# Performance work log

Hardware: AMD Instinct MI355X
Metric: run time of the kernel (lower is better)

Reference implementation:

```python
import jax, jax.numpy as jnp
import numpy as np
import math

D_HEAD = 64
D_MODEL = 1024
N_HEADS = D_MODEL // D_HEAD
MAX_TOKENS = 2048
BATCH = 4
SEQ = 2048


def setup_inputs() -> dict:
    key = jax.random.key(0)
    k1, k2, k3, k4, k5 = jax.random.split(key, 5)
    residual_stream = jax.random.normal(k1, (BATCH, SEQ, D_MODEL), dtype=jnp.float32)
    # kaiming_normal_ (fan_in = d_model for [head, d_model, d_head] with default mode)
    std_qkv = math.sqrt(2.0 / D_MODEL)
    weight_query = jax.random.normal(k2, (N_HEADS, D_MODEL, D_HEAD), dtype=jnp.float32) * std_qkv
    weight_key = jax.random.normal(k3, (N_HEADS, D_MODEL, D_HEAD), dtype=jnp.float32) * std_qkv
    weight_value = jax.random.normal(k4, (N_HEADS, D_MODEL, D_HEAD), dtype=jnp.float32) * std_qkv
    # xavier_normal_ for [d_model, d_model]
    std_out = math.sqrt(2.0 / (D_MODEL + D_MODEL))
    weight_out = jax.random.normal(k5, (D_MODEL, D_MODEL), dtype=jnp.float32) * std_out
    return {
        "residual_stream": residual_stream,
        "weight_query": weight_query,
        "weight_key": weight_key,
        "weight_value": weight_value,
        "weight_out": weight_out,
    }


def reference(residual_stream, weight_query, weight_key, weight_value, weight_out):
    # residual_stream: [b, s, m]; weights: [h, m, d]
    q = jnp.einsum("bsm,hmd->bhsd", residual_stream, weight_query)
    k = jnp.einsum("bsm,hmd->bhsd", residual_stream, weight_key)
    v = jnp.einsum("bsm,hmd->bhsd", residual_stream, weight_value)
    scores = jnp.einsum("bhqd,bhkd->bhqk", q, k) / math.sqrt(D_HEAD)  # [b,h,s,s]
    n = scores.shape[-1]
    causal = jnp.tril(jnp.ones((n, n), dtype=bool))
    scores = jnp.where(causal, scores, -jnp.inf)
    attn = jax.nn.softmax(scores, axis=-1)
    out = jnp.einsum("bhqk,bhkd->bhqd", attn, v)  # [b,h,s,d]
    b, h, s, d = out.shape
    concat = out.transpose(0, 2, 1, 3).reshape(b, s, h * d)  # [b,s,m]
    return jnp.einsum("bsm,mn->bsn", concat, weight_out)
```

## Files before the change

### kernel.cpp

```cpp
#include <hip/hip_runtime.h>
#include <hip/hip_bf16.h>
#include <math.h>

#define BATCH 4
#define SEQ   2048
#define DM    1024
#define NH    16
#define DH    64

#define QSCALE 0.1803368801111204f

typedef __bf16 bf16x8 __attribute__((ext_vector_type(8)));
typedef __bf16 bf16x4 __attribute__((ext_vector_type(4)));
typedef float  f32x4  __attribute__((ext_vector_type(4)));

__device__ __forceinline__ bf16x8 load8f(const float* __restrict__ base, size_t idx) {
    const float4 a = *(const float4*)(base + idx);
    const float4 b = *(const float4*)(base + idx + 4);
    bf16x8 r;
    r[0] = (__bf16)a.x; r[1] = (__bf16)a.y; r[2] = (__bf16)a.z; r[3] = (__bf16)a.w;
    r[4] = (__bf16)b.x; r[5] = (__bf16)b.y; r[6] = (__bf16)b.z; r[7] = (__bf16)b.w;
    return r;
}

__global__ __launch_bounds__(256)
void xconv_kernel(const float* __restrict__ X, __bf16* __restrict__ Xb)
{
    size_t idx = ((size_t)blockIdx.x * 256 + threadIdx.x) * 8;
    *(bf16x8*)&Xb[idx] = load8f(X, idx);
}

__global__ __launch_bounds__(256)
void wtrans_kernel(const float* __restrict__ src, __bf16* __restrict__ dst,
                   int K, int N)
{
    const int k0 = blockIdx.x * 64;
    const int n0 = blockIdx.y * 64;
    src += (size_t)blockIdx.z * K * N;
    dst += (size_t)blockIdx.z * K * N;

    __shared__ __bf16 T[64][65];
    const int t = threadIdx.x;

#pragma unroll
    for (int i = 0; i < 4; ++i) {
        int row = i * 16 + (t >> 4);
        int col = (t & 15) * 4;
        float4 v = *(const float4*)&src[(size_t)(k0 + row) * N + n0 + col];
        T[col + 0][row] = (__bf16)v.x;
        T[col + 1][row] = (__bf16)v.y;
        T[col + 2][row] = (__bf16)v.z;
        T[col + 3][row] = (__bf16)v.w;
    }
    __syncthreads();
#pragma unroll
    for (int i = 0; i < 4; ++i) {
        int n  = i * 16 + (t >> 4);
        int kc = (t & 15) * 4;
        bf16x4 v;
        v[0] = T[n][kc + 0]; v[1] = T[n][kc + 1];
        v[2] = T[n][kc + 2]; v[3] = T[n][kc + 3];
        *(bf16x4*)&dst[(size_t)(n0 + n) * K + k0 + kc] = v;
    }
}

__global__ __launch_bounds__(256)
void qkv_kernel(const __bf16* __restrict__ Xb,
                const __bf16* __restrict__ Wqt,
                const __bf16* __restrict__ Wkt,
                const __bf16* __restrict__ Wvt,
                __bf16* __restrict__ Qo,
                __bf16* __restrict__ Ko,
                __bf16* __restrict__ Vto)
{
    const int rowTile = blockIdx.x;
    const int h       = blockIdx.y;
    const size_t woff = (size_t)h * DH * DM;

    __shared__ __align__(16) __bf16 As[128 * 40];
    __shared__ __align__(16) __bf16 Bq[64 * 40];
    __shared__ __align__(16) __bf16 Bk[64 * 40];
    __shared__ __align__(16) __bf16 Bv[64 * 40];

    const int t    = threadIdx.x;
    const int wave = t >> 6;
    const int lane = t & 63;
    const int l15  = lane & 15;
    const int quad = lane >> 4;

    f32x4 aq[2][4], ak[2][4], av[2][4];
#pragma unroll
    for (int s = 0; s < 2; ++s)
#pragma unroll
        for (int i = 0; i < 4; ++i) {
            aq[s][i] = (f32x4){0.f, 0.f, 0.f, 0.f};
            ak[s][i] = (f32x4){0.f, 0.f, 0.f, 0.f};
            av[s][i] = (f32x4){0.f, 0.f, 0.f, 0.f};
        }

    const int r0    = rowTile * 128;
    const int a_row = t >> 1;
    const int a_col = (t & 1) * 16;
    const int b_row = t >> 2;
    const int b_col = (t & 3) * 8;

    for (int k0 = 0; k0 < DM; k0 += 32) {
        __syncthreads();
        *(bf16x8*)&As[a_row * 40 + a_col] =
            *(const bf16x8*)&Xb[(size_t)(r0 + a_row) * DM + k0 + a_col];
        *(bf16x8*)&As[a_row * 40 + a_col + 8] =
            *(const bf16x8*)&Xb[(size_t)(r0 + a_row) * DM + k0 + a_col + 8];
        *(bf16x8*)&Bq[b_row * 40 + b_col] =
            *(const bf16x8*)&Wqt[woff + (size_t)b_row * DM + k0 + b_col];
        *(bf16x8*)&Bk[b_row * 40 + b_col] =
            *(const bf16x8*)&Wkt[woff + (size_t)b_row * DM + k0 + b_col];
        *(bf16x8*)&Bv[b_row * 40 + b_col] =
            *(const bf16x8*)&Wvt[woff + (size_t)b_row * DM + k0 + b_col];
        __syncthreads();

        bf16x8 a0 = *(const bf16x8*)&As[(wave * 16 + l15) * 40 + quad * 8];
        bf16x8 a1 = *(const bf16x8*)&As[(64 + wave * 16 + l15) * 40 + quad * 8];
#pragma unroll
        for (int ct = 0; ct < 4; ++ct) {
            bf16x8 bq = *(const bf16x8*)&Bq[(ct * 16 + l15) * 40 + quad * 8];
            aq[0][ct] = __builtin_amdgcn_mfma_f32_16x16x32_bf16(a0, bq, aq[0][ct], 0, 0, 0);
            aq[1][ct] = __builtin_amdgcn_mfma_f32_16x16x32_bf16(a1, bq, aq[1][ct], 0, 0, 0);
            bf16x8 bk = *(const bf16x8*)&Bk[(ct * 16 + l15) * 40 + quad * 8];
            ak[0][ct] = __builtin_amdgcn_mfma_f32_16x16x32_bf16(a0, bk, ak[0][ct], 0, 0, 0);
            ak[1][ct] = __builtin_amdgcn_mfma_f32_16x16x32_bf16(a1, bk, ak[1][ct], 0, 0, 0);
            bf16x8 bv = *(const bf16x8*)&Bv[(ct * 16 + l15) * 40 + quad * 8];
            av[0][ct] = __builtin_amdgcn_mfma_f32_16x16x32_bf16(a0, bv, av[0][ct], 0, 0, 0);
            av[1][ct] = __builtin_amdgcn_mfma_f32_16x16x32_bf16(a1, bv, av[1][ct], 0, 0, 0);
        }
    }

#pragma unroll
    for (int st = 0; st < 2; ++st) {
        const int rbase = r0 + st * 64 + wave * 16 + quad * 4;
        const int b = rbase >> 11;
        const int s = rbase & (SEQ - 1);
        const size_t bh = (size_t)(b * NH + h);
#pragma unroll
        for (int ct = 0; ct < 4; ++ct) {
            const int d = ct * 16 + l15;
#pragma unroll
            for (int reg = 0; reg < 4; ++reg) {
                Qo[(bh * SEQ + s + reg) * DH + d] = (__bf16)(aq[st][ct][reg] * QSCALE);
                Ko[(bh * SEQ + s + reg) * DH + d] = (__bf16)ak[st][ct][reg];
            }
            bf16x4 vv;
            vv[0] = (__bf16)av[st][ct][0]; vv[1] = (__bf16)av[st][ct][1];
            vv[2] = (__bf16)av[st][ct][2]; vv[3] = (__bf16)av[st][ct][3];
            *(bf16x4*)&Vto[(bh * DH + d) * SEQ + s] = vv;
        }
    }
}

__global__ __launch_bounds__(256)
void attn_kernel(const __bf16* __restrict__ Q,
                 const __bf16* __restrict__ K,
                 const __bf16* __restrict__ Vt,
                 __bf16* __restrict__ Cat)
{
    const int x   = blockIdx.x;
    const int qtA = x;
    const int qtB = 31 - x;
    const int bh  = blockIdx.y;
    const int b   = bh >> 4;
    const int h   = bh & 15;

    const __bf16* Qg  = Q  + (size_t)bh * SEQ * DH;
    const __bf16* Kg  = K  + (size_t)bh * SEQ * DH;
    const __bf16* Vtg = Vt + (size_t)bh * DH * SEQ;

    __shared__ __align__(16) __bf16 Ks[64 * 72];
    __shared__ __align__(16) __bf16 Vs[64 * 72];
    __shared__ __align__(16) __bf16 Ps[128 * 72];

    const int t    = threadIdx.x;
    const int wave = t >> 6;
    const int lane = t & 63;
    const int l15  = lane & 15;
    const int quad = lane >> 4;

    bf16x8 qfA[2], qfB[2];
    {
        const size_t rA = (size_t)(qtA * 64 + wave * 16 + l15);
        qfA[0] = *(const bf16x8*)&Qg[rA * DH + quad * 8];
        qfA[1] = *(const bf16x8*)&Qg[rA * DH + 32 + quad * 8];
        const size_t rB = (size_t)(qtB * 64 + wave * 16 + l15);
        qfB[0] = *(const bf16x8*)&Qg[rB * DH + quad * 8];
        qfB[1] = *(const bf16x8*)&Qg[rB * DH + 32 + quad * 8];
    }

    bf16x8 ones;
#pragma unroll
    for (int j = 0; j < 8; ++j) ones[j] = (__bf16)1.0f;

    f32x4 oA[4], oB[4], olA, olB;
#pragma unroll
    for (int ct = 0; ct < 4; ++ct) {
        oA[ct] = (f32x4){0.f, 0.f, 0.f, 0.f};
        oB[ct] = (f32x4){0.f, 0.f, 0.f, 0.f};
    }
    olA = (f32x4){0.f, 0.f, 0.f, 0.f};
    olB = (f32x4){0.f, 0.f, 0.f, 0.f};

    const int srow0 = t >> 3;
    const int scol  = (t & 7) * 8;
    bf16x8 kreg[2], vreg[2];
#pragma unroll
    for (int i = 0; i < 2; ++i) {
        int row = srow0 + i * 32;
        kreg[i] = *(const bf16x8*)&Kg[(size_t)row * DH + scol];
        vreg[i] = *(const bf16x8*)&Vtg[(size_t)row * SEQ + scol];
    }

    auto half_step = [&](const bf16x8* qf, f32x4* o, f32x4& ol,
                         bool diag, int psBase) {
        f32x4 sc[4];
#pragma unroll
        for (int ct = 0; ct < 4; ++ct) {
            sc[ct] = (f32x4){0.f, 0.f, 0.f, 0.f};
            bf16x8 b0 = *(const bf16x8*)&Ks[(ct * 16 + l15) * 72 + quad * 8];
            sc[ct] = __builtin_amdgcn_mfma_f32_16x16x32_bf16(qf[0], b0, sc[ct], 0, 0, 0);
            bf16x8 b1 = *(const bf16x8*)&Ks[(ct * 16 + l15) * 72 + 32 + quad * 8];
            sc[ct] = __builtin_amdgcn_mfma_f32_16x16x32_bf16(qf[1], b1, sc[ct], 0, 0, 0);
        }
        if (diag) {
#pragma unroll
            for (int ct = 0; ct < 4; ++ct)
#pragma unroll
                for (int r = 0; r < 4; ++r) {
                    int qr = wave * 16 + quad * 4 + r;
                    int kc = ct * 16 + l15;
                    if (kc > qr) sc[ct][r] = -INFINITY;
                }
        }
#pragma unroll
        for (int ct = 0; ct < 4; ++ct)
#pragma unroll
            for (int r = 0; r < 4; ++r)
                sc[ct][r] = exp2f(sc[ct][r]);

#pragma unroll
        for (int ct = 0; ct < 4; ++ct)
#pragma unroll
            for (int r = 0; r < 4; ++r)
                Ps[(psBase + wave * 16 + quad * 4 + r) * 72 + ct * 16 + l15] =
                    (__bf16)sc[ct][r];

        bf16x8 af0 = *(const bf16x8*)&Ps[(psBase + wave * 16 + l15) * 72 + quad * 8];
        bf16x8 af1 = *(const bf16x8*)&Ps[(psBase + wave * 16 + l15) * 72 + 32 + quad * 8];

#pragma unroll
        for (int ct = 0; ct < 4; ++ct) {
            bf16x8 v0 = *(const bf16x8*)&Vs[(ct * 16 + l15) * 72 + quad * 8];
            o[ct] = __builtin_amdgcn_mfma_f32_16x16x32_bf16(af0, v0, o[ct], 0, 0, 0);
            bf16x8 v1 = *(const bf16x8*)&Vs[(ct * 16 + l15) * 72 + 32 + quad * 8];
            o[ct] = __builtin_amdgcn_mfma_f32_16x16x32_bf16(af1, v1, o[ct], 0, 0, 0);
        }
        ol = __builtin_amdgcn_mfma_f32_16x16x32_bf16(af0, ones, ol, 0, 0, 0);
        ol = __builtin_amdgcn_mfma_f32_16x16x32_bf16(af1, ones, ol, 0, 0, 0);
    };

    for (int kt = 0; kt <= qtB; ++kt) {
        __syncthreads();
#pragma unroll
        for (int i = 0; i < 2; ++i) {
            int row = srow0 + i * 32;
            *(bf16x8*)&Ks[row * 72 + scol] = kreg[i];
            *(bf16x8*)&Vs[row * 72 + scol] = vreg[i];
        }
        __syncthreads();

        {
            const int kvn = (kt < qtB ? kt + 1 : kt) * 64;
#pragma unroll
            for (int i = 0; i < 2; ++i) {
                int row = srow0 + i * 32;
                kreg[i] = *(const bf16x8*)&Kg[(size_t)(kvn + row) * DH + scol];
                vreg[i] = *(const bf16x8*)&Vtg[(size_t)row * SEQ + kvn + scol];
            }
        }

        half_step(qfB, oB, olB, kt == qtB, 64);
        if (kt <= qtA)
            half_step(qfA, oA, olA, kt == qtA, 0);
    }

#pragma unroll
    for (int ct = 0; ct < 4; ++ct)
#pragma unroll
        for (int r = 0; r < 4; ++r) {
            int rr = wave * 16 + quad * 4 + r;
            int sA = qtA * 64 + rr;
            int sB = qtB * 64 + rr;
            Cat[((size_t)(b * SEQ + sA)) * DM + h * DH + ct * 16 + l15] =
                (__bf16)(oA[ct][r] / olA[r]);
            Cat[((size_t)(b * SEQ + sB)) * DM + h * DH + ct * 16 + l15] =
                (__bf16)(oB[ct][r] / olB[r]);
        }
}

__global__ __launch_bounds__(256)
void oproj_kernel(const __bf16* __restrict__ A,
                  const __bf16* __restrict__ Wot,
                  float* __restrict__ C)
{
    const int rowTile = blockIdx.x;
    const int colTile = blockIdx.y;
    const int r0 = rowTile * 128;
    const int n0 = colTile * 128;

    __shared__ __align__(16) __bf16 As[128 * 40];
    __shared__ __align__(16) __bf16 Bs[128 * 40];

    const int t    = threadIdx.x;
    const int wave = t >> 6;
    const int lane = t & 63;
    const int l15  = lane & 15;
    const int quad = lane >> 4;

    f32x4 acc[2][8];
#pragma unroll
    for (int s = 0; s < 2; ++s)
#pragma unroll
        for (int i = 0; i < 8; ++i) acc[s][i] = (f32x4){0.f, 0.f, 0.f, 0.f};

    const int a_row = t >> 1;
    const int a_col = (t & 1) * 16;

    for (int k0 = 0; k0 < DM; k0 += 32) {
        __syncthreads();
        *(bf16x8*)&As[a_row * 40 + a_col] =
            *(const bf16x8*)&A[(size_t)(r0 + a_row) * DM + k0 + a_col];
        *(bf16x8*)&As[a_row * 40 + a_col + 8] =
            *(const bf16x8*)&A[(size_t)(r0 + a_row) * DM + k0 + a_col + 8];
        *(bf16x8*)&Bs[a_row * 40 + a_col] =
            *(const bf16x8*)&Wot[(size_t)(n0 + a_row) * DM + k0 + a_col];
        *(bf16x8*)&Bs[a_row * 40 + a_col + 8] =
            *(const bf16x8*)&Wot[(size_t)(n0 + a_row) * DM + k0 + a_col + 8];
        __syncthreads();

        bf16x8 a0 = *(const bf16x8*)&As[(wave * 16 + l15) * 40 + quad * 8];
        bf16x8 a1 = *(const bf16x8*)&As[(64 + wave * 16 + l15) * 40 + quad * 8];
#pragma unroll
        for (int ct = 0; ct < 8; ++ct) {
            bf16x8 bb = *(const bf16x8*)&Bs[(ct * 16 + l15) * 40 + quad * 8];
            acc[0][ct] = __builtin_amdgcn_mfma_f32_16x16x32_bf16(a0, bb, acc[0][ct], 0, 0, 0);
            acc[1][ct] = __builtin_amdgcn_mfma_f32_16x16x32_bf16(a1, bb, acc[1][ct], 0, 0, 0);
        }
    }

#pragma unroll
    for (int st = 0; st < 2; ++st)
#pragma unroll
        for (int ct = 0; ct < 8; ++ct)
#pragma unroll
            for (int reg = 0; reg < 4; ++reg) {
                int r = r0 + st * 64 + wave * 16 + quad * 4 + reg;
                int n = n0 + ct * 16 + l15;
                C[(size_t)r * DM + n] = acc[st][ct][reg];
            }
}

extern "C" void kernel_launch(void* const* d_in, const int* in_sizes, int n_in,
                              void* d_out, int out_size, void* d_ws, size_t ws_size,
                              hipStream_t stream)
{
    (void)in_sizes; (void)n_in; (void)out_size; (void)ws_size;
    const float* X  = (const float*)d_in[0];
    const float* Wq = (const float*)d_in[1];
    const float* Wk = (const float*)d_in[2];
    const float* Wv = (const float*)d_in[3];
    const float* Wo = (const float*)d_in[4];
    float* out = (float*)d_out;

    char* ws = (char*)d_ws;
    const size_t wqkv_b = (size_t)NH * DM * DH * sizeof(__bf16);
    const size_t wo_b   = (size_t)DM * DM * sizeof(__bf16);
    const size_t big_b  = (size_t)BATCH * NH * SEQ * DH * sizeof(__bf16);
    __bf16* Wqt = (__bf16*)(ws);
    __bf16* Wkt = (__bf16*)(ws + wqkv_b);
    __bf16* Wvt = (__bf16*)(ws + 2 * wqkv_b);
    __bf16* Wot = (__bf16*)(ws + 3 * wqkv_b);
    __bf16* Qb  = (__bf16*)(ws + 3 * wqkv_b + wo_b);
    __bf16* Kb  = (__bf16*)(ws + 3 * wqkv_b + wo_b + big_b);
    __bf16* Vtb = (__bf16*)(ws + 3 * wqkv_b + wo_b + 2 * big_b);
    __bf16* Cat = (__bf16*)(ws + 3 * wqkv_b + wo_b + 3 * big_b);
    __bf16* Xb  = (__bf16*)(ws + 3 * wqkv_b + wo_b + 4 * big_b);

    xconv_kernel<<<dim3(4096), 256, 0, stream>>>(X, Xb);
    wtrans_kernel<<<dim3(16, 1, 16), 256, 0, stream>>>(Wq, Wqt, DM, DH);
    wtrans_kernel<<<dim3(16, 1, 16), 256, 0, stream>>>(Wk, Wkt, DM, DH);
    wtrans_kernel<<<dim3(16, 1, 16), 256, 0, stream>>>(Wv, Wvt, DM, DH);
    wtrans_kernel<<<dim3(16, 16, 1), 256, 0, stream>>>(Wo, Wot, DM, DM);
    qkv_kernel<<<dim3(64, 16), 256, 0, stream>>>(Xb, Wqt, Wkt, Wvt, Qb, Kb, Vtb);
    attn_kernel<<<dim3(16, 64), 256, 0, stream>>>(Qb, Kb, Vtb, Cat);
    oproj_kernel<<<dim3(64, 8), 256, 0, stream>>>(Cat, Wot, out);
}
```

Before: 307.9 us.

## Replace LDS-staged GEMMs with direct register double-buffered loads; split QKV kernel

The QKV and output-projection GEMMs no longer stage tiles through shared memory with barriers. Each wave now loads its MFMA fragments straight from global memory into registers, double-buffered across two k-steps. The fused QKV kernel is also split into a Q/K kernel and a separate V kernel, which lowers register pressure per kernel. This removes syncthreads and LDS traffic, but each wave now loads the weight fragments on its own, so global/L2 traffic rises and the 16-byte-per-lane row-strided loads may coalesce poorly. The split also reads X twice.

```diff
diff --git a/kernel.cpp b/kernel.cpp
--- a/kernel.cpp
+++ b/kernel.cpp
@@ -65,73 +65,65 @@
 }
 
 __global__ __launch_bounds__(256)
-void qkv_kernel(const __bf16* __restrict__ Xb,
-                const __bf16* __restrict__ Wqt,
-                const __bf16* __restrict__ Wkt,
-                const __bf16* __restrict__ Wvt,
-                __bf16* __restrict__ Qo,
-                __bf16* __restrict__ Ko,
-                __bf16* __restrict__ Vto)
+void qk_kernel(const __bf16* __restrict__ Xb,
+               const __bf16* __restrict__ Wqt,
+               const __bf16* __restrict__ Wkt,
+               __bf16* __restrict__ Qo,
+               __bf16* __restrict__ Ko)
 {
     const int rowTile = blockIdx.x;
     const int h       = blockIdx.y;
-    const size_t woff = (size_t)h * DH * DM;
-
-    __shared__ __align__(16) __bf16 As[128 * 40];
-    __shared__ __align__(16) __bf16 Bq[64 * 40];
-    __shared__ __align__(16) __bf16 Bk[64 * 40];
-    __shared__ __align__(16) __bf16 Bv[64 * 40];
 
     const int t    = threadIdx.x;
     const int wave = t >> 6;
     const int lane = t & 63;
     const int l15  = lane & 15;
     const int quad = lane >> 4;
-
-    f32x4 aq[2][4], ak[2][4], av[2][4];
+    const int qoff = quad * 8;
+
+    const int r0 = rowTile * 128;
+    const size_t row0 = (size_t)(r0 + wave * 16 + l15) * DM;
+    const size_t row1 = (size_t)(r0 + 64 + wave * 16 + l15) * DM;
+    const __bf16* Wq = Wqt + (size_t)h * DH * DM;
+    const __bf16* Wk = Wkt + (size_t)h * DH * DM;
+
+    f32x4 aq[2][4], ak[2][4];
 #pragma unroll
     for (int s = 0; s < 2; ++s)
 #pragma unroll
         for (int i = 0; i < 4; ++i) {
             aq[s][i] = (f32x4){0.f, 0.f, 0.f, 0.f};
             ak[s][i] = (f32x4){0.f, 0.f, 0.f, 0.f};
-            av[s][i] = (f32x4){0.f, 0.f, 0.f, 0.f};
-        }
-
-    const int r0    = rowTile * 128;
-    const int a_row = t >> 1;
-    const int a_col = (t & 1) * 16;
-    const int b_row = t >> 2;
-    const int b_col = (t & 3) * 8;
-
-    for (int k0 = 0; k0 < DM; k0 += 32) {
-        __syncthreads();
-        *(bf16x8*)&As[a_row * 40 + a_col] =
-            *(const bf16x8*)&Xb[(size_t)(r0 + a_row) * DM + k0 + a_col];
-        *(bf16x8*)&As[a_row * 40 + a_col + 8] =
-            *(const bf16x8*)&Xb[(size_t)(r0 + a_row) * DM + k0 + a_col + 8];
-        *(bf16x8*)&Bq[b_row * 40 + b_col] =
-            *(const bf16x8*)&Wqt[woff + (size_t)b_row * DM + k0 + b_col];
-        *(bf16x8*)&Bk[b_row * 40 + b_col] =
-            *(const bf16x8*)&Wkt[woff + (size_t)b_row * DM + k0 + b_col];
-        *(bf16x8*)&Bv[b_row * 40 + b_col] =
-            *(const bf16x8*)&Wvt[woff + (size_t)b_row * DM + k0 + b_col];
-        __syncthreads();
-
-        bf16x8 a0 = *(const bf16x8*)&As[(wave * 16 + l15) * 40 + quad * 8];
-        bf16x8 a1 = *(const bf16x8*)&As[(64 + wave * 16 + l15) * 40 + quad * 8];
-#pragma unroll
-        for (int ct = 0; ct < 4; ++ct) {
-            bf16x8 bq = *(const bf16x8*)&Bq[(ct * 16 + l15) * 40 + quad * 8];
-            aq[0][ct] = __builtin_amdgcn_mfma_f32_16x16x32_bf16(a0, bq, aq[0][ct], 0, 0, 0);
-            aq[1][ct] = __builtin_amdgcn_mfma_f32_16x16x32_bf16(a1, bq, aq[1][ct], 0, 0, 0);
-            bf16x8 bk = *(const bf16x8*)&Bk[(ct * 16 + l15) * 40 + quad * 8];
-            ak[0][ct] = __builtin_amdgcn_mfma_f32_16x16x32_bf16(a0, bk, ak[0][ct], 0, 0, 0);
-            ak[1][ct] = __builtin_amdgcn_mfma_f32_16x16x32_bf16(a1, bk, ak[1][ct], 0, 0, 0);
-            bf16x8 bv = *(const bf16x8*)&Bv[(ct * 16 + l15) * 40 + quad * 8];
-            av[0][ct] = __builtin_amdgcn_mfma_f32_16x16x32_bf16(a0, bv, av[0][ct], 0, 0, 0);
-            av[1][ct] = __builtin_amdgcn_mfma_f32_16x16x32_bf16(a1, bv, av[1][ct], 0, 0, 0);
-        }
+        }
+
+    bf16x8 aF[2][2], qF[2][4], kF[2][4];
+
+    auto loadk = [&](int buf, int k0) {
+        aF[buf][0] = *(const bf16x8*)&Xb[row0 + k0 + qoff];
+        aF[buf][1] = *(const bf16x8*)&Xb[row1 + k0 + qoff];
+#pragma unroll
+        for (int ct = 0; ct < 4; ++ct) {
+            const size_t wrow = (size_t)(ct * 16 + l15) * DM + k0 + qoff;
+            qF[buf][ct] = *(const bf16x8*)&Wq[wrow];
+            kF[buf][ct] = *(const bf16x8*)&Wk[wrow];
+        }
+    };
+    auto mfmak = [&](int buf) {
+#pragma unroll
+        for (int ct = 0; ct < 4; ++ct) {
+            aq[0][ct] = __builtin_amdgcn_mfma_f32_16x16x32_bf16(aF[buf][0], qF[buf][ct], aq[0][ct], 0, 0, 0);
+            aq[1][ct] = __builtin_amdgcn_mfma_f32_16x16x32_bf16(aF[buf][1], qF[buf][ct], aq[1][ct], 0, 0, 0);
+            ak[0][ct] = __builtin_amdgcn_mfma_f32_16x16x32_bf16(aF[buf][0], kF[buf][ct], ak[0][ct], 0, 0, 0);
+            ak[1][ct] = __builtin_amdgcn_mfma_f32_16x16x32_bf16(aF[buf][1], kF[buf][ct], ak[1][ct], 0, 0, 0);
+        }
+    };
+
+    loadk(0, 0);
+    for (int k0 = 0; k0 < DM; k0 += 64) {
+        loadk(1, k0 + 32);
+        mfmak(0);
+        loadk(0, (k0 + 64 < DM) ? k0 + 64 : 0);
+        mfmak(1);
     }
 
 #pragma unroll
@@ -148,6 +140,69 @@
                 Qo[(bh * SEQ + s + reg) * DH + d] = (__bf16)(aq[st][ct][reg] * QSCALE);
                 Ko[(bh * SEQ + s + reg) * DH + d] = (__bf16)ak[st][ct][reg];
             }
+        }
+    }
+}
+
+__global__ __launch_bounds__(256)
+void v_kernel(const __bf16* __restrict__ Xb,
+              const __bf16* __restrict__ Wvt,
+              __bf16* __restrict__ Vto)
+{
+    const int rowTile = blockIdx.x;
+    const int h       = blockIdx.y;
+
+    const int t    = threadIdx.x;
+    const int wave = t >> 6;
+    const int lane = t & 63;
+    const int l15  = lane & 15;
+    const int quad = lane >> 4;
+    const int qoff = quad * 8;
+
+    const int r0 = rowTile * 128;
+    const size_t row0 = (size_t)(r0 + wave * 16 + l15) * DM;
+    const size_t row1 = (size_t)(r0 + 64 + wave * 16 + l15) * DM;
+    const __bf16* Wv = Wvt + (size_t)h * DH * DM;
+
+    f32x4 av[2][4];
+#pragma unroll
+    for (int s = 0; s < 2; ++s)
+#pragma unroll
+        for (int i = 0; i < 4; ++i) av[s][i] = (f32x4){0.f, 0.f, 0.f, 0.f};
+
+    bf16x8 aF[2][2], vF[2][4];
+    auto loadk = [&](int buf, int k0) {
+        aF[buf][0] = *(const bf16x8*)&Xb[row0 + k0 + qoff];
+        aF[buf][1] = *(const bf16x8*)&Xb[row1 + k0 + qoff];
+#pragma unroll
+        for (int ct = 0; ct < 4; ++ct)
+            vF[buf][ct] = *(const bf16x8*)&Wv[(size_t)(ct * 16 + l15) * DM + k0 + qoff];
+    };
+    auto mfmak = [&](int buf) {
+#pragma unroll
+        for (int ct = 0; ct < 4; ++ct) {
+            av[0][ct] = __builtin_amdgcn_mfma_f32_16x16x32_bf16(aF[buf][0], vF[buf][ct], av[0][ct], 0, 0, 0);
+            av[1][ct] = __builtin_amdgcn_mfma_f32_16x16x32_bf16(aF[buf][1], vF[buf][ct], av[1][ct], 0, 0, 0);
+        }
+    };
+
+    loadk(0, 0);
+    for (int k0 = 0; k0 < DM; k0 += 64) {
+        loadk(1, k0 + 32);
+        mfmak(0);
+        loadk(0, (k0 + 64 < DM) ? k0 + 64 : 0);
+        mfmak(1);
+    }
+
+#pragma unroll
+    for (int st = 0; st < 2; ++st) {
+        const int rbase = r0 + st * 64 + wave * 16 + quad * 4;
+        const int b = rbase >> 11;
+        const int s = rbase & (SEQ - 1);
+        const size_t bh = (size_t)(b * NH + h);
+#pragma unroll
+        for (int ct = 0; ct < 4; ++ct) {
+            const int d = ct * 16 + l15;
             bf16x4 vv;
             vv[0] = (__bf16)av[st][ct][0]; vv[1] = (__bf16)av[st][ct][1];
             vv[2] = (__bf16)av[st][ct][2]; vv[3] = (__bf16)av[st][ct][3];
@@ -313,14 +368,15 @@
     const int r0 = rowTile * 128;
     const int n0 = colTile * 128;
 
-    __shared__ __align__(16) __bf16 As[128 * 40];
-    __shared__ __align__(16) __bf16 Bs[128 * 40];
-
     const int t    = threadIdx.x;
     const int wave = t >> 6;
     const int lane = t & 63;
     const int l15  = lane & 15;
     const int quad = lane >> 4;
+    const int qoff = quad * 8;
+
+    const size_t row0 = (size_t)(r0 + wave * 16 + l15) * DM;
+    const size_t row1 = (size_t)(r0 + 64 + wave * 16 + l15) * DM;
 
     f32x4 acc[2][8];
 #pragma unroll
@@ -328,29 +384,28 @@
 #pragma unroll
         for (int i = 0; i < 8; ++i) acc[s][i] = (f32x4){0.f, 0.f, 0.f, 0.f};
 
-    const int a_row = t >> 1;
-    const int a_col = (t & 1) * 16;
-
-    for (int k0 = 0; k0 < DM; k0 += 32) {
-        __syncthreads();
-        *(bf16x8*)&As[a_row * 40 + a_col] =
-            *(const bf16x8*)&A[(size_t)(r0 + a_row) * DM + k0 + a_col];
-        *(bf16x8*)&As[a_row * 40 + a_col + 8] =
-            *(const bf16x8*)&A[(size_t)(r0 + a_row) * DM + k0 + a_col + 8];
-        *(bf16x8*)&Bs[a_row * 40 + a_col] =
-            *(const bf16x8*)&Wot[(size_t)(n0 + a_row) * DM + k0 + a_col];
-        *(bf16x8*)&Bs[a_row * 40 + a_col + 8] =
-            *(const bf16x8*)&Wot[(size_t)(n0 + a_row) * DM + k0 + a_col + 8];
-        __syncthreads();
-
-        bf16x8 a0 = *(const bf16x8*)&As[(wave * 16 + l15) * 40 + quad * 8];
-        bf16x8 a1 = *(const bf16x8*)&As[(64 + wave * 16 + l15) * 40 + quad * 8];
+    bf16x8 aF[2][2], bF[2][8];
+    auto loadk = [&](int buf, int k0) {
+        aF[buf][0] = *(const bf16x8*)&A[row0 + k0 + qoff];
+        aF[buf][1] = *(const bf16x8*)&A[row1 + k0 + qoff];
+#pragma unroll
+        for (int ct = 0; ct < 8; ++ct)
+            bF[buf][ct] = *(const bf16x8*)&Wot[(size_t)(n0 + ct * 16 + l15) * DM + k0 + qoff];
+    };
+    auto mfmak = [&](int buf) {
 #pragma unroll
         for (int ct = 0; ct < 8; ++ct) {
-            bf16x8 bb = *(const bf16x8*)&Bs[(ct * 16 + l15) * 40 + quad * 8];
-            acc[0][ct] = __builtin_amdgcn_mfma_f32_16x16x32_bf16(a0, bb, acc[0][ct], 0, 0, 0);
-            acc[1][ct] = __builtin_amdgcn_mfma_f32_16x16x32_bf16(a1, bb, acc[1][ct], 0, 0, 0);
-        }
+            acc[0][ct] = __builtin_amdgcn_mfma_f32_16x16x32_bf16(aF[buf][0], bF[buf][ct], acc[0][ct], 0, 0, 0);
+            acc[1][ct] = __builtin_amdgcn_mfma_f32_16x16x32_bf16(aF[buf][1], bF[buf][ct], acc[1][ct], 0, 0, 0);
+        }
+    };
+
+    loadk(0, 0);
+    for (int k0 = 0; k0 < DM; k0 += 64) {
+        loadk(1, k0 + 32);
+        mfmak(0);
+        loadk(0, (k0 + 64 < DM) ? k0 + 64 : 0);
+        mfmak(1);
     }
 
 #pragma unroll
@@ -396,7 +451,8 @@
     wtrans_kernel<<<dim3(16, 1, 16), 256, 0, stream>>>(Wk, Wkt, DM, DH);
     wtrans_kernel<<<dim3(16, 1, 16), 256, 0, stream>>>(Wv, Wvt, DM, DH);
     wtrans_kernel<<<dim3(16, 16, 1), 256, 0, stream>>>(Wo, Wot, DM, DM);
-    qkv_kernel<<<dim3(64, 16), 256, 0, stream>>>(Xb, Wqt, Wkt, Wvt, Qb, Kb, Vtb);
+    qk_kernel<<<dim3(64, 16), 256, 0, stream>>>(Xb, Wqt, Wkt, Qb, Kb);
+    v_kernel<<<dim3(64, 16), 256, 0, stream>>>(Xb, Wvt, Vtb);
     attn_kernel<<<dim3(16, 64), 256, 0, stream>>>(Qb, Kb, Vtb, Cat);
     oproj_kernel<<<dim3(64, 8), 256, 0, stream>>>(Cat, Wot, out);
 }
```

Result: slower. 514.6 us (+67.1%).
